# Performance work log

Measured on AMD Instinct MI355X. Metric: run time of the kernel, lower is better.

## Reference

```python
import jax, jax.numpy as jnp
import numpy as np

HIDDEN = 1024

def setup_inputs() -> dict:
    key = jax.random.key(0)
    ks = jax.random.split(key, 8)
    B, Ti, Tt, V, H, U, K = 4, 2048, 2048, 32000, 1024, 4096, 3
    return {
        "inputs": jax.random.randint(ks[0], (B, Ti), 0, V, dtype=jnp.int32),
        "targets": jax.random.randint(ks[1], (B, Tt), 0, V, dtype=jnp.int32),
        "input_emb": jax.random.normal(ks[2], (V, H), jnp.float32) * 0.02,
        "target_emb": jax.random.normal(ks[3], (V, H), jnp.float32) * 0.02,
        "conv_w": jax.random.normal(ks[4], (K, H, U), jnp.float32) * 0.02,
        "conv_b": jnp.zeros((U,), jnp.float32),
        "dense_w": jax.random.normal(ks[5], (U, H), jnp.float32) * 0.02,
        "dense_b": jnp.zeros((H,), jnp.float32),
    }

def reference(inputs, targets, input_emb, target_emb, conv_w, conv_b, dense_w, dense_b):
    emb_scale = jnp.asarray(HIDDEN, jnp.float32) ** 0.5
    # EmbeddingSharedWeights: gather + sqrt(hidden) scaling
    ie = jnp.take(input_emb, inputs, axis=0) * emb_scale    # [B, Ti, H]
    te = jnp.take(target_emb, targets, axis=0) * emb_scale  # [B, Tt, H]
    # manual scaled dot-product cross-attention (no masks: defaults are None)
    dk = jnp.asarray(ie.shape[-1], jnp.float32)
    logits = jnp.einsum("btd,bsd->bts", te, ie) / jnp.sqrt(dk)  # [B, Tt, Ti]
    weights = jax.nn.softmax(logits, axis=-1)
    attn = jnp.einsum("bts,bsd->btd", weights, ie)              # [B, Tt, H]
    # LanguageModel: Conv1D(units, kernel_size, same) + relu + Dense(hidden)
    h = jax.lax.conv_general_dilated(
        attn, conv_w, window_strides=(1,), padding="SAME",
        dimension_numbers=("NWC", "WIO", "NWC")) + conv_b        # [B, Tt, U]
    h = jax.nn.relu(h)
    out = jnp.einsum("btu,uh->bth", h, dense_w) + dense_b       # [B, Tt, H]
    return out
```

## Files before the change

### kernel.cpp

```cpp
#include <hip/hip_runtime.h>
#include <cstddef>

static constexpr int HID = 1024;
static constexpr int NB  = 4;
static constexpr int TT  = 2048;
static constexpr int UD  = 4096;
static constexpr int PR  = TT + 1;

typedef short bf8    __attribute__((ext_vector_type(8)));
typedef float f32x4  __attribute__((ext_vector_type(4)));

__device__ __forceinline__ unsigned short f2bf(float x) {
  unsigned int u = __float_as_uint(x);
  u += 0x7fffu + ((u >> 16) & 1u);
  return (unsigned short)(u >> 16);
}
__device__ __forceinline__ float bf2f(unsigned short h) {
  return __uint_as_float(((unsigned int)h) << 16);
}
__device__ __forceinline__ unsigned short cvt_bf(float x) { return f2bf(x); }
__device__ __forceinline__ unsigned short cvt_bf(unsigned short x) { return x; }

__device__ __forceinline__ void g2l16(const unsigned short* g, unsigned short* l) {
  __builtin_amdgcn_global_load_lds(
      (const __attribute__((address_space(1))) unsigned int*)g,
      (__attribute__((address_space(3))) unsigned int*)l, 16, 0, 0);
}

#define BARX() __builtin_amdgcn_s_barrier()
#define VMCNT(n) asm volatile("s_waitcnt vmcnt(" #n ")" ::: "memory")

__global__ __launch_bounds__(256) void gather_split_k(
    const int* __restrict__ idx, const float* __restrict__ emb,
    unsigned short* __restrict__ hi, unsigned short* __restrict__ lo, float scale)
{
  const int row = blockIdx.x;
  const int r = idx[row];
  const int c = threadIdx.x * 4;
  float4 v = *(const float4*)(emb + (size_t)r * HID + c);
  v.x *= scale; v.y *= scale; v.z *= scale; v.w *= scale;
  ushort4 h, l;
  h.x = f2bf(v.x); h.y = f2bf(v.y); h.z = f2bf(v.z); h.w = f2bf(v.w);
  l.x = f2bf(v.x - bf2f(h.x)); l.y = f2bf(v.y - bf2f(h.y));
  l.z = f2bf(v.z - bf2f(h.z)); l.w = f2bf(v.w - bf2f(h.w));
  *(ushort4*)(hi + (size_t)row * HID + c) = h;
  *(ushort4*)(lo + (size_t)row * HID + c) = l;
}

__global__ __launch_bounds__(256) void zero_guard_k(unsigned short* __restrict__ p)
{
  unsigned short* row = p + (size_t)blockIdx.x * PR * HID;
  *(ushort4*)(row + threadIdx.x * 4) = (ushort4){0, 0, 0, 0};
}

template<typename TIN>
__global__ __launch_bounds__(256) void transpose_bf_k(
    const TIN* __restrict__ in, unsigned short* __restrict__ out,
    int R, int C, long long sIn, long long sOut)
{
  __shared__ unsigned short tile[32][33];
  in  += (size_t)blockIdx.z * sIn;
  out += (size_t)blockIdx.z * sOut;
  const int r0 = blockIdx.y * 32, c0 = blockIdx.x * 32;
  const int tc = threadIdx.x & 31, tr8 = threadIdx.x >> 5;
#pragma unroll
  for (int p = 0; p < 4; ++p) {
    const int r = tr8 + p * 8;
    tile[r][tc] = cvt_bf(in[(size_t)(r0 + r) * C + c0 + tc]);
  }
  __syncthreads();
#pragma unroll
  for (int p = 0; p < 4; ++p) {
    const int c = tr8 + p * 8;
    out[(size_t)(c0 + c) * R + r0 + tc] = tile[tc][c];
  }
}

__global__ __launch_bounds__(256) void softmax_bf_k(
    const float* __restrict__ L, unsigned short* __restrict__ W)
{
  const float* row = L + (size_t)blockIdx.x * TT;
  unsigned short* wout = W + (size_t)blockIdx.x * TT;
  const int tid = threadIdx.x;
  float4 v0 = ((const float4*)row)[tid * 2];
  float4 v1 = ((const float4*)row)[tid * 2 + 1];
  float mx = fmaxf(fmaxf(fmaxf(v0.x, v0.y), fmaxf(v0.z, v0.w)),
                   fmaxf(fmaxf(v1.x, v1.y), fmaxf(v1.z, v1.w)));
#pragma unroll
  for (int off = 32; off > 0; off >>= 1)
    mx = fmaxf(mx, __shfl_xor(mx, off, 64));
  __shared__ float sred[8];
  const int wid = tid >> 6;
  if ((tid & 63) == 0) sred[wid] = mx;
  __syncthreads();
  mx = fmaxf(fmaxf(sred[0], sred[1]), fmaxf(sred[2], sred[3]));
  v0.x = __expf(v0.x - mx); v0.y = __expf(v0.y - mx);
  v0.z = __expf(v0.z - mx); v0.w = __expf(v0.w - mx);
  v1.x = __expf(v1.x - mx); v1.y = __expf(v1.y - mx);
  v1.z = __expf(v1.z - mx); v1.w = __expf(v1.w - mx);
  float s = v0.x + v0.y + v0.z + v0.w + v1.x + v1.y + v1.z + v1.w;
#pragma unroll
  for (int off = 32; off > 0; off >>= 1)
    s += __shfl_xor(s, off, 64);
  if ((tid & 63) == 0) sred[4 + wid] = s;
  __syncthreads();
  s = sred[4] + sred[5] + sred[6] + sred[7];
  const float inv = 1.0f / s;
  ushort4 o0, o1;
  o0.x = f2bf(v0.x * inv); o0.y = f2bf(v0.y * inv);
  o0.z = f2bf(v0.z * inv); o0.w = f2bf(v0.w * inv);
  o1.x = f2bf(v1.x * inv); o1.y = f2bf(v1.y * inv);
  o1.z = f2bf(v1.z * inv); o1.w = f2bf(v1.w * inv);
  *(ushort4*)(wout + tid * 8)     = o0;
  *(ushort4*)(wout + tid * 8 + 4) = o1;
}

template<int CONVA>
__device__ __forceinline__ void stage_half(
    const unsigned short* __restrict__ P, int ld, int r0, int t, int ks,
    unsigned short* lds, int tid)
{
  const int bk = t * 64 + ks * 32;
  const int ke = (((tid & 3) ^ ((tid >> 3) & 3)) << 3);
  int rowbase, kcol;
  if constexpr (CONVA) {
    const int seg = bk >> 10;
    kcol = (bk & 1023) + ke;
    rowbase = r0 + (tid >> 2) + seg - 1;
  } else {
    kcol = bk + ke;
    rowbase = r0 + (tid >> 2);
  }
#pragma unroll
  for (int c = 0; c < 2; ++c)
    g2l16(P + (ptrdiff_t)(rowbase + c * 128) * ld + kcol,
          lds + c * 4096 + tid * 8);
}

template<int OUTBF, int EPI, int CONVA>
__global__ __launch_bounds__(512, 2) void gemm256_k(
    const unsigned short* __restrict__ A, long long sA, int lda,
    const unsigned short* __restrict__ B, long long sB, int ldb,
    void* __restrict__ Cv, long long sC, int ldc,
    int K, const float* __restrict__ bias)
{
  __shared__ __align__(16) unsigned short As[2][2][256 * 32];
  __shared__ __align__(16) unsigned short Bs[2][2][256 * 32];
  const int tid = threadIdx.x;
  A += (size_t)blockIdx.z * sA;
  B += (size_t)blockIdx.z * sB;
  const int bm = blockIdx.y * 256;
  const int bn = blockIdx.x * 256;
  const int wave = tid >> 6, lane = tid & 63;
  const int wr = wave >> 2, wcn = wave & 3;
  const int q = lane >> 4, l16 = lane & 15;
  const int ksw = ((q ^ ((l16 >> 1) & 3)) << 3);
  const int abase = (wr * 128 + l16) * 32 + ksw;
  const int bbase = (wcn * 64 + l16) * 32 + ksw;

  f32x4 acc[8][4];
#pragma unroll
  for (int i = 0; i < 8; ++i)
#pragma unroll
    for (int j = 0; j < 4; ++j)
      acc[i][j] = (f32x4){0.f, 0.f, 0.f, 0.f};

  const int T = K >> 6;

  stage_half<CONVA>(A, lda, bm, 0, 0, &As[0][0][0], tid);
  stage_half<0>   (B, ldb, bn, 0, 0, &Bs[0][0][0], tid);
  stage_half<CONVA>(A, lda, bm, 0, 1, &As[0][1][0], tid);
  stage_half<0>   (B, ldb, bn, 0, 1, &Bs[0][1][0], tid);
  VMCNT(4);
  BARX();

  bf8 af[4], bfr[4];
  for (int t = 0; t < T; ++t) {
    const int buf = t & 1;
    unsigned short* An0 = &As[buf ^ 1][0][0];
    unsigned short* An1 = &As[buf ^ 1][1][0];
    unsigned short* Bn0 = &Bs[buf ^ 1][0][0];
    unsigned short* Bn1 = &Bs[buf ^ 1][1][0];
    const bool next = (t + 1 < T);

#pragma unroll
    for (int j = 0; j < 4; ++j) bfr[j] = *(const bf8*)&Bs[buf][0][bbase + j * 512];
#pragma unroll
    for (int m = 0; m < 4; ++m) af[m] = *(const bf8*)&As[buf][0][abase + m * 512];
    if (next) stage_half<CONVA>(A, lda, bm, t + 1, 0, An0, tid);
    BARX();
    __builtin_amdgcn_s_setprio(1);
#pragma unroll
    for (int m = 0; m < 4; ++m)
#pragma unroll
      for (int j = 0; j < 4; ++j)
        acc[m][j] = __builtin_amdgcn_mfma_f32_16x16x32_bf16(af[m], bfr[j], acc[m][j], 0, 0, 0);
    __builtin_amdgcn_s_setprio(0);
    BARX();

#pragma unroll
    for (int m = 0; m < 4; ++m) af[m] = *(const bf8*)&As[buf][0][abase + (4 + m) * 512];
    if (next) { stage_half<0>(B, ldb, bn, t + 1, 0, Bn0, tid); VMCNT(4); }
    else      { VMCNT(0); }
    BARX();
    __builtin_amdgcn_s_setprio(1);
#pragma unroll
    for (int m = 0; m < 4; ++m)
#pragma unroll
      for (int j = 0; j < 4; ++j)
        acc[4 + m][j] = __builtin_amdgcn_mfma_f32_16x16x32_bf16(af[m], bfr[j], acc[4 + m][j], 0, 0, 0);
    __builtin_amdgcn_s_setprio(0);
    BARX();

#pragma unroll
    for (int j = 0; j < 4; ++j) bfr[j] = *(const bf8*)&Bs[buf][1][bbase + j * 512];
#pragma unroll
    for (int m = 0; m < 4; ++m) af[m] = *(const bf8*)&As[buf][1][abase + m * 512];
    if (next) stage_half<CONVA>(A, lda, bm, t + 1, 1, An1, tid);
    BARX();
    __builtin_amdgcn_s_setprio(1);
#pragma unroll
    for (int m = 0; m < 4; ++m)
#pragma unroll
      for (int j = 0; j < 4; ++j)
        acc[m][j] = __builtin_amdgcn_mfma_f32_16x16x32_bf16(af[m], bfr[j], acc[m][j], 0, 0, 0);
    __builtin_amdgcn_s_setprio(0);
    BARX();

#pragma unroll
    for (int m = 0; m < 4; ++m) af[m] = *(const bf8*)&As[buf][1][abase + (4 + m) * 512];
    if (next) { stage_half<0>(B, ldb, bn, t + 1, 1, Bn1, tid); VMCNT(4); }
    BARX();
    __builtin_amdgcn_s_setprio(1);
#pragma unroll
    for (int m = 0; m < 4; ++m)
#pragma unroll
      for (int j = 0; j < 4; ++j)
        acc[4 + m][j] = __builtin_amdgcn_mfma_f32_16x16x32_bf16(af[m], bfr[j], acc[4 + m][j], 0, 0, 0);
    __builtin_amdgcn_s_setprio(0);
    BARX();
  }

  float* Cf          = (float*)Cv          + (size_t)blockIdx.z * sC;
  unsigned short* Cb = (unsigned short*)Cv + (size_t)blockIdx.z * sC;
#pragma unroll
  for (int j = 0; j < 4; ++j) {
    const int col = bn + wcn * 64 + j * 16 + l16;
    float bv = 0.f;
    if constexpr (EPI >= 1) bv = bias[col];
#pragma unroll
    for (int i = 0; i < 8; ++i) {
      const int row0 = bm + wr * 128 + i * 16 + q * 4;
#pragma unroll
      for (int r = 0; r < 4; ++r) {
        float v = acc[i][j][r];
        if constexpr (EPI >= 1) v += bv;
        if constexpr (EPI == 2) v = fmaxf(v, 0.f);
        if constexpr (OUTBF) Cb[(size_t)(row0 + r) * ldc + col] = f2bf(v);
        else                 Cf[(size_t)(row0 + r) * ldc + col] = v;
      }
    }
  }
}

__global__ __launch_bounds__(256) void gemm_logits_k(
    const unsigned short* __restrict__ Ah, const unsigned short* __restrict__ Al,
    const unsigned short* __restrict__ Bh, const unsigned short* __restrict__ Bl,
    float* __restrict__ C)
{
  __shared__ unsigned short AsH[4 * 128 * 8], AsL[4 * 128 * 8];
  __shared__ unsigned short BsH[4 * 128 * 8], BsL[4 * 128 * 8];
  const int tid = threadIdx.x;
  const long long SE = (long long)TT * HID;
  Ah += (size_t)blockIdx.z * SE; Al += (size_t)blockIdx.z * SE;
  Bh += (size_t)blockIdx.z * SE; Bl += (size_t)blockIdx.z * SE;
  C  += (size_t)blockIdx.z * TT * TT;
  const int bm = blockIdx.y * 128;
  const int bn = blockIdx.x * 128;
  const int wave = tid >> 6, lane = tid & 63;
  const int wr = wave >> 1, wc = wave & 1;
  const int q = lane >> 4, l16 = lane & 15;
  const int sr  = tid & 127;
  const int skb = tid >> 7;

  f32x4 acc[4][4];
#pragma unroll
  for (int i = 0; i < 4; ++i)
#pragma unroll
    for (int j = 0; j < 4; ++j)
      acc[i][j] = (f32x4){0.f, 0.f, 0.f, 0.f};

  for (int k0 = 0; k0 < HID; k0 += 32) {
#pragma unroll
    for (int h = 0; h < 2; ++h) {
      const int kb = skb + h * 2;
      const int kk = k0 + kb * 8;
      const size_t ao = (size_t)(bm + sr) * HID + kk;
      const size_t bo = (size_t)(bn + sr) * HID + kk;
      const int lo = (kb * 128 + sr) * 8;
      g2l16(Ah + ao, &AsH[lo]);
      g2l16(Al + ao, &AsL[lo]);
      g2l16(Bh + bo, &BsH[lo]);
      g2l16(Bl + bo, &BsL[lo]);
    }
    __syncthreads();
    bf8 ah[4], al[4], bh[4], bl[4];
#pragma unroll
    for (int i = 0; i < 4; ++i) {
      const int lo = (q * 128 + wr * 64 + i * 16 + l16) * 8;
      ah[i] = *(const bf8*)&AsH[lo];
      al[i] = *(const bf8*)&AsL[lo];
    }
#pragma unroll
    for (int j = 0; j < 4; ++j) {
      const int lo = (q * 128 + wc * 64 + j * 16 + l16) * 8;
      bh[j] = *(const bf8*)&BsH[lo];
      bl[j] = *(const bf8*)&BsL[lo];
    }
#pragma unroll
    for (int i = 0; i < 4; ++i)
#pragma unroll
      for (int j = 0; j < 4; ++j) {
        acc[i][j] = __builtin_amdgcn_mfma_f32_16x16x32_bf16(ah[i], bh[j], acc[i][j], 0, 0, 0);
        acc[i][j] = __builtin_amdgcn_mfma_f32_16x16x32_bf16(ah[i], bl[j], acc[i][j], 0, 0, 0);
        acc[i][j] = __builtin_amdgcn_mfma_f32_16x16x32_bf16(al[i], bh[j], acc[i][j], 0, 0, 0);
      }
    __syncthreads();
  }

#pragma unroll
  for (int j = 0; j < 4; ++j) {
    const int col = bn + wc * 64 + j * 16 + l16;
#pragma unroll
    for (int i = 0; i < 4; ++i) {
      const int row0 = bm + wr * 64 + i * 16 + q * 4;
#pragma unroll
      for (int r = 0; r < 4; ++r)
        C[(size_t)(row0 + r) * TT + col] = acc[i][j][r];
    }
  }
}

extern "C" void kernel_launch(void* const* d_in, const int* in_sizes, int n_in,
                              void* d_out, int out_size, void* d_ws, size_t ws_size,
                              hipStream_t stream)
{
  const int*   inputs     = (const int*)d_in[0];
  const int*   targets    = (const int*)d_in[1];
  const float* input_emb  = (const float*)d_in[2];
  const float* target_emb = (const float*)d_in[3];
  const float* conv_w     = (const float*)d_in[4];
  const float* conv_b     = (const float*)d_in[5];
  const float* dense_w    = (const float*)d_in[6];
  const float* dense_b    = (const float*)d_in[7];
  float* out = (float*)d_out;

  const long long SE = (long long)TT * HID;
  const size_t SZ = (size_t)NB * SE * 2;

  char* base = (char*)d_ws;
  unsigned short* te_hi = (unsigned short*)(base);
  unsigned short* te_lo = (unsigned short*)(base + SZ);
  unsigned short* ie_hi = (unsigned short*)(base + 2 * SZ);
  unsigned short* ie_lo = (unsigned short*)(base + 3 * SZ);
  float*          logit = (float*)         (base + 4 * SZ);
  unsigned short* Wbf   = (unsigned short*)(base + 4 * SZ + (size_t)NB * TT * TT * 4);
  unsigned short* ieT     = (unsigned short*)(base);
  unsigned short* attnP   = (unsigned short*)(base + SZ);
  unsigned short* attnD   = attnP + (size_t)HID;
  unsigned short* convwb  = (unsigned short*)(base + 2 * SZ + 16384);
  unsigned short* hb      = (unsigned short*)(base + 4 * SZ);
  unsigned short* densewb = (unsigned short*)Wbf;

  gather_split_k<<<NB * TT, 256, 0, stream>>>(targets, target_emb, te_hi, te_lo, 1.0f);
  gather_split_k<<<NB * TT, 256, 0, stream>>>(inputs,  input_emb,  ie_hi, ie_lo, 32.0f);

  gemm_logits_k<<<dim3(TT / 128, TT / 128, NB), 256, 0, stream>>>(
      te_hi, te_lo, ie_hi, ie_lo, logit);

  transpose_bf_k<unsigned short><<<dim3(HID / 32, TT / 32, NB), 256, 0, stream>>>(
      ie_hi, ieT, TT, HID, SE, SE);

  softmax_bf_k<<<NB * TT, 256, 0, stream>>>(logit, Wbf);

  zero_guard_k<<<NB + 1, 256, 0, stream>>>(attnP);
  gemm256_k<1, 0, 0><<<dim3(HID / 256, TT / 256, NB), 512, 0, stream>>>(
      Wbf, (long long)TT * TT, TT, ieT, SE, TT,
      attnD, (long long)PR * HID, HID, TT, nullptr);

  transpose_bf_k<float><<<dim3(UD / 32, (3 * HID) / 32, 1), 256, 0, stream>>>(
      conv_w, convwb, 3 * HID, UD, 0, 0);
  transpose_bf_k<float><<<dim3(HID / 32, UD / 32, 1), 256, 0, stream>>>(
      dense_w, densewb, UD, HID, 0, 0);

  gemm256_k<1, 2, 1><<<dim3(UD / 256, TT / 256, NB), 512, 0, stream>>>(
      attnD, (long long)PR * HID, HID, convwb, 0, 3 * HID,
      hb, (long long)TT * UD, UD, 3 * HID, conv_b);

  gemm256_k<0, 1, 0><<<dim3(HID / 256, TT / 256, NB), 512, 0, stream>>>(
      hb, (long long)TT * UD, UD, densewb, 0, UD,
      out, SE, HID, UD, dense_b);
}
```

Measured before the change: 831.7 us.

## Retile logits GEMM to 256x256 pipelined, add 128-row GEMM and XCD swizzle

```diff
diff --git a/kernel.cpp b/kernel.cpp
--- a/kernel.cpp
+++ b/kernel.cpp
@@ -29,6 +29,16 @@
 
 #define BARX() __builtin_amdgcn_s_barrier()
 #define VMCNT(n) asm volatile("s_waitcnt vmcnt(" #n ")" ::: "memory")
+
+__device__ __forceinline__ void xcd_swz(int& bx, int& by, int& bz) {
+  const int gx = gridDim.x, gy = gridDim.y;
+  const int nwg = gx * gy * (int)gridDim.z;
+  int flat = bx + gx * (by + gy * bz);
+  const int cpx = nwg >> 3;
+  flat = (flat & 7) * cpx + (flat >> 3);
+  bx = flat % gx; flat /= gx;
+  by = flat % gy; bz = flat / gy;
+}
 
 __global__ __launch_bounds__(256) void gather_split_k(
     const int* __restrict__ idx, const float* __restrict__ emb,
@@ -115,6 +125,24 @@
   *(ushort4*)(wout + tid * 8 + 4) = o1;
 }
 
+__device__ __forceinline__ void stage256(
+    const unsigned short* __restrict__ P, int ld, int r0, int kk,
+    unsigned short* lds, int tid)
+{
+  const int ke = (((tid & 3) ^ ((tid >> 3) & 3)) << 3);
+  const int row = r0 + (tid >> 2);
+  g2l16(P + (size_t)row * ld + kk + ke, lds + tid * 8);
+  g2l16(P + (size_t)(row + 128) * ld + kk + ke, lds + 4096 + tid * 8);
+}
+__device__ __forceinline__ void stage128(
+    const unsigned short* __restrict__ P, int ld, int r0, int kk,
+    unsigned short* lds, int tid)
+{
+  const int ke = (((tid & 3) ^ ((tid >> 3) & 3)) << 3);
+  const int row = r0 + (tid >> 2);
+  g2l16(P + (size_t)row * ld + kk + ke, lds + tid * 8);
+}
+
 template<int CONVA>
 __device__ __forceinline__ void stage_half(
     const unsigned short* __restrict__ P, int ld, int r0, int t, int ks,
@@ -147,10 +175,12 @@
   __shared__ __align__(16) unsigned short As[2][2][256 * 32];
   __shared__ __align__(16) unsigned short Bs[2][2][256 * 32];
   const int tid = threadIdx.x;
-  A += (size_t)blockIdx.z * sA;
-  B += (size_t)blockIdx.z * sB;
-  const int bm = blockIdx.y * 256;
-  const int bn = blockIdx.x * 256;
+  int bxi = blockIdx.x, byi = blockIdx.y, bzi = blockIdx.z;
+  xcd_swz(bxi, byi, bzi);
+  A += (size_t)bzi * sA;
+  B += (size_t)bzi * sB;
+  const int bm = byi * 256;
+  const int bn = bxi * 256;
   const int wave = tid >> 6, lane = tid & 63;
   const int wr = wave >> 2, wcn = wave & 3;
   const int q = lane >> 4, l16 = lane & 15;
@@ -241,8 +271,8 @@
     BARX();
   }
 
-  float* Cf          = (float*)Cv          + (size_t)blockIdx.z * sC;
-  unsigned short* Cb = (unsigned short*)Cv + (size_t)blockIdx.z * sC;
+  float* Cf          = (float*)Cv          + (size_t)bzi * sC;
+  unsigned short* Cb = (unsigned short*)Cv + (size_t)bzi * sC;
 #pragma unroll
   for (int j = 0; j < 4; ++j) {
     const int col = bn + wcn * 64 + j * 16 + l16;
@@ -263,77 +293,227 @@
   }
 }
 
-__global__ __launch_bounds__(256) void gemm_logits_k(
+template<int OUTBF, int EPI>
+__global__ __launch_bounds__(512, 2) void gemm128_k(
+    const unsigned short* __restrict__ A, long long sA, int lda,
+    const unsigned short* __restrict__ B, long long sB, int ldb,
+    void* __restrict__ Cv, long long sC, int ldc,
+    int K, const float* __restrict__ bias)
+{
+  __shared__ __align__(16) unsigned short As[2][2][128 * 32];
+  __shared__ __align__(16) unsigned short Bs[2][2][256 * 32];
+  const int tid = threadIdx.x;
+  int bxi = blockIdx.x, byi = blockIdx.y, bzi = blockIdx.z;
+  xcd_swz(bxi, byi, bzi);
+  A += (size_t)bzi * sA;
+  B += (size_t)bzi * sB;
+  const int bm = byi * 128;
+  const int bn = bxi * 256;
+  const int wave = tid >> 6, lane = tid & 63;
+  const int wr = wave >> 2, wcn = wave & 3;
+  const int q = lane >> 4, l16 = lane & 15;
+  const int ksw = ((q ^ ((l16 >> 1) & 3)) << 3);
+  const int abase = (wr * 64 + l16) * 32 + ksw;
+  const int bbase = (wcn * 64 + l16) * 32 + ksw;
+
+  f32x4 acc[4][4];
+#pragma unroll
+  for (int i = 0; i < 4; ++i)
+#pragma unroll
+    for (int j = 0; j < 4; ++j)
+      acc[i][j] = (f32x4){0.f, 0.f, 0.f, 0.f};
+
+  const int T = K >> 6;
+
+  stage128(A, lda, bm, 0,  &As[0][0][0], tid);
+  stage256(B, ldb, bn, 0,  &Bs[0][0][0], tid);
+  stage128(A, lda, bm, 32, &As[0][1][0], tid);
+  stage256(B, ldb, bn, 32, &Bs[0][1][0], tid);
+  VMCNT(3);
+  BARX();
+
+  bf8 af[4], bfr[4];
+  for (int t = 0; t < T; ++t) {
+    const int buf = t & 1;
+    const bool next = (t + 1 < T);
+    const int kk = (t + 1) * 64;
+
+#pragma unroll
+    for (int j = 0; j < 4; ++j) bfr[j] = *(const bf8*)&Bs[buf][0][bbase + j * 512];
+#pragma unroll
+    for (int m = 0; m < 4; ++m) af[m] = *(const bf8*)&As[buf][0][abase + m * 512];
+    if (next) {
+      stage128(A, lda, bm, kk,      &As[buf ^ 1][0][0], tid);
+      stage256(B, ldb, bn, kk,      &Bs[buf ^ 1][0][0], tid);
+      VMCNT(3);
+    } else { VMCNT(0); }
+    BARX();
+    __builtin_amdgcn_s_setprio(1);
+#pragma unroll
+    for (int m = 0; m < 4; ++m)
+#pragma unroll
+      for (int j = 0; j < 4; ++j)
+        acc[m][j] = __builtin_amdgcn_mfma_f32_16x16x32_bf16(af[m], bfr[j], acc[m][j], 0, 0, 0);
+    __builtin_amdgcn_s_setprio(0);
+    BARX();
+
+#pragma unroll
+    for (int j = 0; j < 4; ++j) bfr[j] = *(const bf8*)&Bs[buf][1][bbase + j * 512];
+#pragma unroll
+    for (int m = 0; m < 4; ++m) af[m] = *(const bf8*)&As[buf][1][abase + m * 512];
+    if (next) {
+      stage128(A, lda, bm, kk + 32, &As[buf ^ 1][1][0], tid);
+      stage256(B, ldb, bn, kk + 32, &Bs[buf ^ 1][1][0], tid);
+      VMCNT(3);
+    }
+    BARX();
+    __builtin_amdgcn_s_setprio(1);
+#pragma unroll
+    for (int m = 0; m < 4; ++m)
+#pragma unroll
+      for (int j = 0; j < 4; ++j)
+        acc[m][j] = __builtin_amdgcn_mfma_f32_16x16x32_bf16(af[m], bfr[j], acc[m][j], 0, 0, 0);
+    __builtin_amdgcn_s_setprio(0);
+    BARX();
+  }
+
+  float* Cf          = (float*)Cv          + (size_t)bzi * sC;
+  unsigned short* Cb = (unsigned short*)Cv + (size_t)bzi * sC;
+#pragma unroll
+  for (int j = 0; j < 4; ++j) {
+    const int col = bn + wcn * 64 + j * 16 + l16;
+    float bv = 0.f;
+    if constexpr (EPI >= 1) bv = bias[col];
+#pragma unroll
+    for (int i = 0; i < 4; ++i) {
+      const int row0 = bm + wr * 64 + i * 16 + q * 4;
+#pragma unroll
+      for (int r = 0; r < 4; ++r) {
+        float v = acc[i][j][r];
+        if constexpr (EPI >= 1) v += bv;
+        if constexpr (EPI == 2) v = fmaxf(v, 0.f);
+        if constexpr (OUTBF) Cb[(size_t)(row0 + r) * ldc + col] = f2bf(v);
+        else                 Cf[(size_t)(row0 + r) * ldc + col] = v;
+      }
+    }
+  }
+}
+
+__global__ __launch_bounds__(512, 2) void gemm_logits256_k(
     const unsigned short* __restrict__ Ah, const unsigned short* __restrict__ Al,
     const unsigned short* __restrict__ Bh, const unsigned short* __restrict__ Bl,
     float* __restrict__ C)
 {
-  __shared__ unsigned short AsH[4 * 128 * 8], AsL[4 * 128 * 8];
-  __shared__ unsigned short BsH[4 * 128 * 8], BsL[4 * 128 * 8];
+  __shared__ __align__(16) unsigned short AsH[2][256 * 32];
+  __shared__ __align__(16) unsigned short AsL[2][256 * 32];
+  __shared__ __align__(16) unsigned short BsH[2][256 * 32];
+  __shared__ __align__(16) unsigned short BsL[2][256 * 32];
   const int tid = threadIdx.x;
+  int bxi = blockIdx.x, byi = blockIdx.y, bzi = blockIdx.z;
+  xcd_swz(bxi, byi, bzi);
   const long long SE = (long long)TT * HID;
-  Ah += (size_t)blockIdx.z * SE; Al += (size_t)blockIdx.z * SE;
-  Bh += (size_t)blockIdx.z * SE; Bl += (size_t)blockIdx.z * SE;
-  C  += (size_t)blockIdx.z * TT * TT;
-  const int bm = blockIdx.y * 128;
-  const int bn = blockIdx.x * 128;
+  Ah += (size_t)bzi * SE; Al += (size_t)bzi * SE;
+  Bh += (size_t)bzi * SE; Bl += (size_t)bzi * SE;
+  C  += (size_t)bzi * TT * TT;
+  const int bm = byi * 256;
+  const int bn = bxi * 256;
   const int wave = tid >> 6, lane = tid & 63;
-  const int wr = wave >> 1, wc = wave & 1;
+  const int wr = wave >> 2, wcn = wave & 3;
   const int q = lane >> 4, l16 = lane & 15;
-  const int sr  = tid & 127;
-  const int skb = tid >> 7;
-
-  f32x4 acc[4][4];
-#pragma unroll
-  for (int i = 0; i < 4; ++i)
+  const int ksw = ((q ^ ((l16 >> 1) & 3)) << 3);
+  const int abase = (wr * 128 + l16) * 32 + ksw;
+  const int bbase = (wcn * 64 + l16) * 32 + ksw;
+
+  f32x4 acc[8][4];
+#pragma unroll
+  for (int i = 0; i < 8; ++i)
 #pragma unroll
     for (int j = 0; j < 4; ++j)
       acc[i][j] = (f32x4){0.f, 0.f, 0.f, 0.f};
 
-  for (int k0 = 0; k0 < HID; k0 += 32) {
-#pragma unroll
-    for (int h = 0; h < 2; ++h) {
-      const int kb = skb + h * 2;
-      const int kk = k0 + kb * 8;
-      const size_t ao = (size_t)(bm + sr) * HID + kk;
-      const size_t bo = (size_t)(bn + sr) * HID + kk;
-      const int lo = (kb * 128 + sr) * 8;
-      g2l16(Ah + ao, &AsH[lo]);
-      g2l16(Al + ao, &AsL[lo]);
-      g2l16(Bh + bo, &BsH[lo]);
-      g2l16(Bl + bo, &BsL[lo]);
-    }
-    __syncthreads();
-    bf8 ah[4], al[4], bh[4], bl[4];
-#pragma unroll
-    for (int i = 0; i < 4; ++i) {
-      const int lo = (q * 128 + wr * 64 + i * 16 + l16) * 8;
-      ah[i] = *(const bf8*)&AsH[lo];
-      al[i] = *(const bf8*)&AsL[lo];
-    }
-#pragma unroll
-    for (int j = 0; j < 4; ++j) {
-      const int lo = (q * 128 + wc * 64 + j * 16 + l16) * 8;
-      bh[j] = *(const bf8*)&BsH[lo];
-      bl[j] = *(const bf8*)&BsL[lo];
-    }
-#pragma unroll
-    for (int i = 0; i < 4; ++i)
+  const int T = HID / 32;
+
+  stage256(Ah, HID, bm, 0, &AsH[0][0], tid);
+  stage256(Bh, HID, bn, 0, &BsH[0][0], tid);
+  stage256(Al, HID, bm, 0, &AsL[0][0], tid);
+  stage256(Bl, HID, bn, 0, &BsL[0][0], tid);
+  VMCNT(4);
+  BARX();
+
+  bf8 bh[4], bl[4], a0[4], a1[4], a2[4], a3[4];
+  for (int t = 0; t < T; ++t) {
+    const int buf = t & 1;
+    const bool next = (t + 1 < T);
+    const int kk = (t + 1) * 32;
+
+#pragma unroll
+    for (int j = 0; j < 4; ++j) bh[j] = *(const bf8*)&BsH[buf][bbase + j * 512];
+#pragma unroll
+    for (int m = 0; m < 4; ++m) a0[m] = *(const bf8*)&AsH[buf][abase + m * 512];
+    if (next) stage256(Ah, HID, bm, kk, &AsH[buf ^ 1][0], tid);
+    BARX();
+    __builtin_amdgcn_s_setprio(1);
+#pragma unroll
+    for (int m = 0; m < 4; ++m)
+#pragma unroll
+      for (int j = 0; j < 4; ++j)
+        acc[m][j] = __builtin_amdgcn_mfma_f32_16x16x32_bf16(a0[m], bh[j], acc[m][j], 0, 0, 0);
+    __builtin_amdgcn_s_setprio(0);
+    BARX();
+
+#pragma unroll
+    for (int m = 0; m < 4; ++m) a1[m] = *(const bf8*)&AsH[buf][abase + (4 + m) * 512];
+    if (next) { stage256(Bh, HID, bn, kk, &BsH[buf ^ 1][0], tid); VMCNT(4); }
+    else      { VMCNT(0); }
+    BARX();
+    __builtin_amdgcn_s_setprio(1);
+#pragma unroll
+    for (int m = 0; m < 4; ++m)
+#pragma unroll
+      for (int j = 0; j < 4; ++j)
+        acc[4 + m][j] = __builtin_amdgcn_mfma_f32_16x16x32_bf16(a1[m], bh[j], acc[4 + m][j], 0, 0, 0);
+    __builtin_amdgcn_s_setprio(0);
+    BARX();
+
+#pragma unroll
+    for (int j = 0; j < 4; ++j) bl[j] = *(const bf8*)&BsL[buf][bbase + j * 512];
+#pragma unroll
+    for (int m = 0; m < 4; ++m) a2[m] = *(const bf8*)&AsL[buf][abase + m * 512];
+    if (next) stage256(Al, HID, bm, kk, &AsL[buf ^ 1][0], tid);
+    BARX();
+    __builtin_amdgcn_s_setprio(1);
+#pragma unroll
+    for (int m = 0; m < 4; ++m)
 #pragma unroll
       for (int j = 0; j < 4; ++j) {
-        acc[i][j] = __builtin_amdgcn_mfma_f32_16x16x32_bf16(ah[i], bh[j], acc[i][j], 0, 0, 0);
-        acc[i][j] = __builtin_amdgcn_mfma_f32_16x16x32_bf16(ah[i], bl[j], acc[i][j], 0, 0, 0);
-        acc[i][j] = __builtin_amdgcn_mfma_f32_16x16x32_bf16(al[i], bh[j], acc[i][j], 0, 0, 0);
+        acc[m][j] = __builtin_amdgcn_mfma_f32_16x16x32_bf16(a0[m], bl[j], acc[m][j], 0, 0, 0);
+        acc[m][j] = __builtin_amdgcn_mfma_f32_16x16x32_bf16(a2[m], bh[j], acc[m][j], 0, 0, 0);
       }
-    __syncthreads();
+    __builtin_amdgcn_s_setprio(0);
+    BARX();
+
+#pragma unroll
+    for (int m = 0; m < 4; ++m) a3[m] = *(const bf8*)&AsL[buf][abase + (4 + m) * 512];
+    if (next) { stage256(Bl, HID, bn, kk, &BsL[buf ^ 1][0], tid); VMCNT(4); }
+    BARX();
+    __builtin_amdgcn_s_setprio(1);
+#pragma unroll
+    for (int m = 0; m < 4; ++m)
+#pragma unroll
+      for (int j = 0; j < 4; ++j) {
+        acc[4 + m][j] = __builtin_amdgcn_mfma_f32_16x16x32_bf16(a1[m], bl[j], acc[4 + m][j], 0, 0, 0);
+        acc[4 + m][j] = __builtin_amdgcn_mfma_f32_16x16x32_bf16(a3[m], bh[j], acc[4 + m][j], 0, 0, 0);
+      }
+    __builtin_amdgcn_s_setprio(0);
+    BARX();
   }
 
 #pragma unroll
   for (int j = 0; j < 4; ++j) {
-    const int col = bn + wc * 64 + j * 16 + l16;
-#pragma unroll
-    for (int i = 0; i < 4; ++i) {
-      const int row0 = bm + wr * 64 + i * 16 + q * 4;
+    const int col = bn + wcn * 64 + j * 16 + l16;
+#pragma unroll
+    for (int i = 0; i < 8; ++i) {
+      const int row0 = bm + wr * 128 + i * 16 + q * 4;
 #pragma unroll
       for (int r = 0; r < 4; ++r)
         C[(size_t)(row0 + r) * TT + col] = acc[i][j][r];
@@ -375,7 +555,7 @@
   gather_split_k<<<NB * TT, 256, 0, stream>>>(targets, target_emb, te_hi, te_lo, 1.0f);
   gather_split_k<<<NB * TT, 256, 0, stream>>>(inputs,  input_emb,  ie_hi, ie_lo, 32.0f);
 
-  gemm_logits_k<<<dim3(TT / 128, TT / 128, NB), 256, 0, stream>>>(
+  gemm_logits256_k<<<dim3(TT / 256, TT / 256, NB), 512, 0, stream>>>(
       te_hi, te_lo, ie_hi, ie_lo, logit);
 
   transpose_bf_k<unsigned short><<<dim3(HID / 32, TT / 32, NB), 256, 0, stream>>>(
@@ -384,7 +564,7 @@
   softmax_bf_k<<<NB * TT, 256, 0, stream>>>(logit, Wbf);
 
   zero_guard_k<<<NB + 1, 256, 0, stream>>>(attnP);
-  gemm256_k<1, 0, 0><<<dim3(HID / 256, TT / 256, NB), 512, 0, stream>>>(
+  gemm128_k<1, 0><<<dim3(HID / 256, TT / 128, NB), 512, 0, stream>>>(
       Wbf, (long long)TT * TT, TT, ieT, SE, TT,
       attnD, (long long)PR * HID, HID, TT, nullptr);
 
@@ -397,7 +577,7 @@
       attnD, (long long)PR * HID, HID, convwb, 0, 3 * HID,
       hb, (long long)TT * UD, UD, 3 * HID, conv_b);
 
-  gemm256_k<0, 1, 0><<<dim3(HID / 256, TT / 256, NB), 512, 0, stream>>>(
+  gemm128_k<0, 1><<<dim3(HID / 256, TT / 128, NB), 512, 0, stream>>>(
       hb, (long long)TT * UD, UD, densewb, 0, UD,
       out, SE, HID, UD, dense_b);
 }
```

Result: faster. 724.5 us (-12.9%).
